# Kernel optimization log

Hardware: AMD Instinct MI355X
Metric: run time of the kernel (lower is better)

The kernel has to match this reference:

```python
import jax, jax.numpy as jnp
import numpy as np

N = 50000      # nodes
E = 800000     # edges (before self loops)
F_IN = 64      # n_features
H = 4          # heads
EPS = 1e-5


def _feast_conv(x, src, dst, W, u, c, b, out_ch):
    # FeaStConv (PyG): q_h = softmax_h(u_h^T (x_j - x_i) + c_h);
    # x_i' = mean_{j in N(i)} sum_h q_h * (W_h x_j) + b
    xs = x[src]                                   # [E', Fin]
    xd = x[dst]                                   # [E', Fin]
    q = jax.nn.softmax((xs - xd) @ u + c, axis=-1)          # [E', H]
    m = (xs @ W).reshape(xs.shape[0], H, out_ch)            # [E', H, out]
    msg = jnp.einsum('eh,eho->eo', q, m)                    # [E', out]
    num = jax.ops.segment_sum(msg, dst, num_segments=N)     # [N, out]
    deg = jax.ops.segment_sum(jnp.ones((msg.shape[0],), msg.dtype), dst, num_segments=N)
    return num / jnp.clip(deg, 1.0)[:, None] + b


def setup_inputs() -> dict:
    key = jax.random.key(0)
    ks = jax.random.split(key, 32)
    def gn(k, shape, s=0.1):
        return jax.random.normal(k, shape, jnp.float32) * s
    inp = {
        'x': jax.random.normal(ks[0], (N, F_IN), jnp.float32),
        'edge_index': jax.random.randint(ks[1], (2, E), 0, N),
        # FeaStConv 1: 64 -> 16
        'W1': gn(ks[2], (F_IN, H * 16)), 'u1': gn(ks[3], (F_IN, H)),
        'c1': gn(ks[4], (H,)), 'b1': gn(ks[5], (16,)),
        # FeaStConv 2: 16 -> 32
        'W2': gn(ks[6], (16, H * 32)), 'u2': gn(ks[7], (16, H)),
        'c2': gn(ks[8], (H,)), 'b2': gn(ks[9], (32,)),
        # FeaStConv 3: 32 -> 64
        'W3': gn(ks[10], (32, H * 64)), 'u3': gn(ks[11], (32, H)),
        'c3': gn(ks[12], (H,)), 'b3': gn(ks[13], (64,)),
        # BatchNorm(64) affine params (training-mode batch stats)
        'gamma': jnp.ones((64,), jnp.float32), 'beta': jnp.zeros((64,), jnp.float32),
        # MLP head
        'lw1': gn(ks[14], (64, 32)), 'lb1': gn(ks[15], (32,)),
        'lw2': gn(ks[16], (32, 16)), 'lb2': gn(ks[17], (16,)),
        'lw3': gn(ks[18], (16, 8)),  'lb3': gn(ks[19], (8,)),
        'lw4': gn(ks[20], (8, 4)),   'lb4': gn(ks[21], (4,)),
        'ow':  gn(ks[22], (4, 1)),   'ob':  gn(ks[23], (1,)),
    }
    return inp


def reference(x, edge_index, W1, u1, c1, b1, W2, u2, c2, b2, W3, u3, c3, b3,
              gamma, beta, lw1, lb1, lw2, lb2, lw3, lb3, lw4, lb4, ow, ob):
    # add self loops (PyG FeaStConv default)
    loops = jnp.arange(N, dtype=edge_index.dtype)
    src = jnp.concatenate([edge_index[0], loops])
    dst = jnp.concatenate([edge_index[1], loops])

    h = jax.nn.relu(_feast_conv(x, src, dst, W1, u1, c1, b1, 16))
    h = jax.nn.relu(_feast_conv(h, src, dst, W2, u2, c2, b2, 32))
    h = jax.nn.relu(_feast_conv(h, src, dst, W3, u3, c3, b3, 64))

    # BatchNorm over node dim (training-mode biased batch stats)
    mu = h.mean(axis=0)
    var = h.var(axis=0)
    h = (h - mu) * jax.lax.rsqrt(var + EPS) * gamma + beta

    h = jax.nn.relu(h @ lw1 + lb1)
    h = jax.nn.relu(h @ lw2 + lb2)
    h = jax.nn.relu(h @ lw3 + lb3)
    h = jax.nn.relu(h @ lw4 + lb4)
    return jax.nn.sigmoid(h @ ow + ob)    # [N, 1]
```

## Files before the change

### kernel.cpp

```cpp
#include <hip/hip_runtime.h>

#define NNODES 50000
#define NEDGES 800000
#define SCAN_BLOCKS ((NNODES + 255) / 256)
#define NPART (NNODES / 8)
#define EPS 2048
#define NSLICE ((NEDGES + EPS - 1) / EPS)

typedef unsigned short u16;

__device__ __forceinline__ float4 softq(float4 ss, float4 sd, float4 c4) {
  float l0 = ss.x - sd.x + c4.x;
  float l1 = ss.y - sd.y + c4.y;
  float l2 = ss.z - sd.z + c4.z;
  float l3 = ss.w - sd.w + c4.w;
  float mx = fmaxf(fmaxf(l0, l1), fmaxf(l2, l3));
  float e0 = __expf(l0 - mx), e1 = __expf(l1 - mx);
  float e2 = __expf(l2 - mx), e3 = __expf(l3 - mx);
  float inv = 1.f / (e0 + e1 + e2 + e3);
  return make_float4(e0 * inv, e1 * inv, e2 * inv, e3 * inv);
}

__device__ __forceinline__ void fma4(float4& a, float q, float4 v) {
  a.x += q * v.x; a.y += q * v.y; a.z += q * v.z; a.w += q * v.w;
}
__device__ __forceinline__ float dot4(float4 a, float4 b) {
  return a.x * b.x + a.y * b.y + a.z * b.z + a.w * b.w;
}
__device__ __forceinline__ void st4T(float* ldsT, int k0, int NBp, int nl, float4 v) {
  ldsT[(k0 + 0) * NBp + nl] = v.x;
  ldsT[(k0 + 1) * NBp + nl] = v.y;
  ldsT[(k0 + 2) * NBp + nl] = v.z;
  ldsT[(k0 + 3) * NBp + nl] = v.w;
}
__device__ __forceinline__ float4 shfl4(float4 v, int e, int w) {
  return make_float4(__shfl(v.x, e, w), __shfl(v.y, e, w),
                     __shfl(v.z, e, w), __shfl(v.w, e, w));
}

__global__ __launch_bounds__(256) void hist_kernel(const int* __restrict__ ei,
                                                   int* __restrict__ counts,
                                                   u16* __restrict__ rank) {
  int e = blockIdx.x * 256 + threadIdx.x;
  if (e < NEDGES) rank[e] = (u16)atomicAdd(&counts[ei[NEDGES + e]], 1);
}

__global__ __launch_bounds__(256) void scanA_kernel(const int* __restrict__ counts,
                                                    int* __restrict__ rowptr,
                                                    int* __restrict__ blockSum) {
  __shared__ int sm[256];
  int i = blockIdx.x * 256 + threadIdx.x;
  int v = (i < NNODES) ? counts[i] : 0;
  sm[threadIdx.x] = v;
  __syncthreads();
  for (int off = 1; off < 256; off <<= 1) {
    int x = (threadIdx.x >= off) ? sm[threadIdx.x - off] : 0;
    __syncthreads();
    sm[threadIdx.x] += x;
    __syncthreads();
  }
  if (i < NNODES) rowptr[i] = sm[threadIdx.x] - v;
  if (threadIdx.x == 255) blockSum[blockIdx.x] = sm[255];
}

__global__ __launch_bounds__(256) void scanBC_kernel(const int* __restrict__ blockSum,
                                                     int* __restrict__ rowptr) {
  __shared__ int sm[256];
  int v = (threadIdx.x < SCAN_BLOCKS) ? blockSum[threadIdx.x] : 0;
  sm[threadIdx.x] = v;
  __syncthreads();
  for (int off = 1; off < 256; off <<= 1) {
    int x = (threadIdx.x >= off) ? sm[threadIdx.x - off] : 0;
    __syncthreads();
    sm[threadIdx.x] += x;
    __syncthreads();
  }
  int off = (blockIdx.x == 0) ? 0 : sm[blockIdx.x - 1];
  int i = blockIdx.x * 256 + threadIdx.x;
  if (i < NNODES) rowptr[i] += off;
  if (i == 0) rowptr[NNODES] = NEDGES;
}

__global__ __launch_bounds__(256) void scatter_kernel(const int* __restrict__ ei,
                                                      const int* __restrict__ rowptr,
                                                      const u16* __restrict__ rank,
                                                      u16* __restrict__ col) {
  const int p = blockIdx.x & 7;
  const int sl = blockIdx.x >> 3;
  const int P0 = p * NPART;
  const int e1 = min((sl + 1) * EPS, NEDGES);
  for (int e = sl * EPS + threadIdx.x; e < e1; e += 256) {
    int dst = __builtin_nontemporal_load(&ei[NEDGES + e]);
    if ((unsigned)(dst - P0) < (unsigned)NPART) {
      int pos = rowptr[dst] + (int)__builtin_nontemporal_load(&rank[e]);
      col[pos] = (u16)__builtin_nontemporal_load(&ei[e]);
    }
  }
}

__global__ __launch_bounds__(256) void prep_kernel(const float* __restrict__ W1,
                                                   const float* __restrict__ W2,
                                                   const float* __restrict__ W3,
                                                   float* __restrict__ Wk1,
                                                   float* __restrict__ Wk2,
                                                   float* __restrict__ Wk3) {
  int i = blockIdx.x * 256 + threadIdx.x;
  if (i < 4096) {
    int f = i >> 6, j = i & 63;
    Wk1[i] = W1[f * 64 + ((j & 3) << 4) + (j >> 2)];
  } else if (i < 6144) {
    int i2 = i - 4096;
    int k = i2 >> 5, o = i2 & 31;
    int hh = k >> 4, f = k & 15;
    Wk2[i2] = W2[f * 128 + hh * 32 + o];
  } else if (i < 14336) {
    int i3 = i - 6144;
    int k = i3 >> 6, o = i3 & 63;
    int hh = k >> 5, f = k & 31;
    Wk3[i3] = W3[f * 256 + hh * 64 + o];
  }
}

template<int K, int OUTT, int MO>
__global__ __launch_bounds__(256) void ngemm_kernel(const float* __restrict__ A,
                                                    const float* __restrict__ Wk,
                                                    float* __restrict__ C) {
  constexpr int OG = OUTT / MO;
  constexpr int NB = 256 / OG;
  constexpr int NBp = NB + 1;
  __shared__ float ldsT[K * NBp];
  const int tid = threadIdx.x;
  const int nb0 = blockIdx.x * NB;
  for (int i = tid; i < NB * (K / 4); i += 256) {
    int r = i / (K / 4), kq = i - r * (K / 4);
    int n = nb0 + r;
    if (n >= NNODES) n = NNODES - 1;
    float4 v = ((const float4*)A)[n * (K / 4) + kq];
    st4T(ldsT, kq << 2, NBp, r, v);
  }
  __syncthreads();
  const int o0 = __builtin_amdgcn_readfirstlane(tid / NB) * MO;
  const int nl = tid & (NB - 1);
  const int n = nb0 + nl;
  float acc[MO];
#pragma unroll
  for (int m = 0; m < MO; ++m) acc[m] = 0.f;
#pragma unroll 4
  for (int k = 0; k < K; ++k) {
    float a = ldsT[k * NBp + nl];
    const float* wr = Wk + k * OUTT + o0;
#pragma unroll
    for (int m = 0; m < MO; ++m) acc[m] += a * wr[m];
  }
  if (n < NNODES) {
#pragma unroll
    for (int m4 = 0; m4 < MO / 4; ++m4) {
      float4 v = make_float4(acc[m4 * 4 + 0], acc[m4 * 4 + 1],
                             acc[m4 * 4 + 2], acc[m4 * 4 + 3]);
      ((float4*)C)[n * (OUTT / 4) + (o0 >> 2) + m4] = v;
    }
  }
}

template<int FIN, int OUTT, int MO>
__global__ __launch_bounds__(256) void fusedG_kernel(const int* __restrict__ rowptr,
                                                     const u16* __restrict__ col,
                                                     const float* __restrict__ s,
                                                     const float* __restrict__ x,
                                                     const float* __restrict__ Wk,
                                                     const float* __restrict__ cptr,
                                                     const float* __restrict__ bptr,
                                                     float* __restrict__ h) {
  constexpr int LPN = FIN / 8;
  constexpr int NB = 256 / LPN;
  constexpr int NBp = NB + 1;
  constexpr int K = 4 * FIN;
  constexpr int OG = OUTT / MO;
  static_assert(OG == 256 / NB, "geometry mismatch");
  __shared__ float ldsT[K * NBp];
  const int tid = threadIdx.x;
  const int nb0 = blockIdx.x * NB;
  const float4* sF4 = (const float4*)s;
  const float4* xF4 = (const float4*)x;

  {
    const int lane = tid & (LPN - 1);
    const int sub = tid / LPN;
    int n = nb0 + sub;
    if (n >= NNODES) n = NNODES - 1;
    float4 c4 = *(const float4*)cptr;
    float mxc = fmaxf(fmaxf(c4.x, c4.y), fmaxf(c4.z, c4.w));
    float4 qsl = make_float4(__expf(c4.x - mxc), __expf(c4.y - mxc),
                             __expf(c4.z - mxc), __expf(c4.w - mxc));
    float sinv = 1.f / (qsl.x + qsl.y + qsl.z + qsl.w);
    qsl.x *= sinv; qsl.y *= sinv; qsl.z *= sinv; qsl.w *= sinv;
    float4 sd = sF4[n];
    const float4* xn = xF4 + n * (FIN / 4) + 2 * lane;
    float4 xa = xn[0], xb = xn[1];
    float4 g0a = make_float4(qsl.x * xa.x, qsl.x * xa.y, qsl.x * xa.z, qsl.x * xa.w);
    float4 g0b = make_float4(qsl.x * xb.x, qsl.x * xb.y, qsl.x * xb.z, qsl.x * xb.w);
    float4 g1a = make_float4(qsl.y * xa.x, qsl.y * xa.y, qsl.y * xa.z, qsl.y * xa.w);
    float4 g1b = make_float4(qsl.y * xb.x, qsl.y * xb.y, qsl.y * xb.z, qsl.y * xb.w);
    float4 g2a = make_float4(qsl.z * xa.x, qsl.z * xa.y, qsl.z * xa.z, qsl.z * xa.w);
    float4 g2b = make_float4(qsl.z * xb.x, qsl.z * xb.y, qsl.z * xb.z, qsl.z * xb.w);
    float4 g3a = make_float4(qsl.w * xa.x, qsl.w * xa.y, qsl.w * xa.z, qsl.w * xa.w);
    float4 g3b = make_float4(qsl.w * xb.x, qsl.w * xb.y, qsl.w * xb.z, qsl.w * xb.w);
    const int beg = rowptr[n], end = rowptr[n + 1];
    int idx = beg;
    for (; idx + LPN <= end; idx += LPN) {
      int myS = (int)col[idx + lane];
      float4 qL = softq(sF4[myS], sd, c4);
#pragma unroll
      for (int e = 0; e < LPN; ++e) {
        int srcE = __shfl(myS, e, LPN);
        float4 q = shfl4(qL, e, LPN);
        const float4* xr = xF4 + srcE * (FIN / 4) + 2 * lane;
        float4 x0a = xr[0], x0b = xr[1];
        fma4(g0a, q.x, x0a); fma4(g0b, q.x, x0b);
        fma4(g1a, q.y, x0a); fma4(g1b, q.y, x0b);
        fma4(g2a, q.z, x0a); fma4(g2b, q.z, x0b);
        fma4(g3a, q.w, x0a); fma4(g3b, q.w, x0b);
      }
    }
    for (; idx < end; ++idx) {
      int s0 = (int)col[idx];
      float4 qv = softq(sF4[s0], sd, c4);
      const float4* xr = xF4 + s0 * (FIN / 4) + 2 * lane;
      float4 x0a = xr[0], x0b = xr[1];
      fma4(g0a, qv.x, x0a); fma4(g0b, qv.x, x0b);
      fma4(g1a, qv.y, x0a); fma4(g1b, qv.y, x0b);
      fma4(g2a, qv.z, x0a); fma4(g2b, qv.z, x0b);
      fma4(g3a, qv.w, x0a); fma4(g3b, qv.w, x0b);
    }
    const int f0 = 8 * lane;
    st4T(ldsT, 0 * FIN + f0, NBp, sub, g0a); st4T(ldsT, 0 * FIN + f0 + 4, NBp, sub, g0b);
    st4T(ldsT, 1 * FIN + f0, NBp, sub, g1a); st4T(ldsT, 1 * FIN + f0 + 4, NBp, sub, g1b);
    st4T(ldsT, 2 * FIN + f0, NBp, sub, g2a); st4T(ldsT, 2 * FIN + f0 + 4, NBp, sub, g2b);
    st4T(ldsT, 3 * FIN + f0, NBp, sub, g3a); st4T(ldsT, 3 * FIN + f0 + 4, NBp, sub, g3b);
  }
  __syncthreads();

  const int o0 = __builtin_amdgcn_readfirstlane(tid / NB) * MO;
  const int nl = tid & (NB - 1);
  const int n = nb0 + nl;
  float acc[MO];
#pragma unroll
  for (int m = 0; m < MO; ++m) acc[m] = 0.f;
#pragma unroll 4
  for (int k = 0; k < K; ++k) {
    float a = ldsT[k * NBp + nl];
    const float* wr = Wk + k * OUTT + o0;
#pragma unroll
    for (int m = 0; m < MO; ++m) acc[m] += a * wr[m];
  }
  if (n < NNODES) {
    float sc = 1.f / (float)(rowptr[n + 1] - rowptr[n] + 1);
#pragma unroll
    for (int m4 = 0; m4 < MO / 4; ++m4) {
      float4 v;
      v.x = fmaxf(acc[m4 * 4 + 0] * sc + bptr[o0 + m4 * 4 + 0], 0.f);
      v.y = fmaxf(acc[m4 * 4 + 1] * sc + bptr[o0 + m4 * 4 + 1], 0.f);
      v.z = fmaxf(acc[m4 * 4 + 2] * sc + bptr[o0 + m4 * 4 + 2], 0.f);
      v.w = fmaxf(acc[m4 * 4 + 3] * sc + bptr[o0 + m4 * 4 + 3], 0.f);
      ((float4*)h)[n * (OUTT / 4) + (o0 >> 2) + m4] = v;
    }
  }
}

template<int FIN>
__global__ __launch_bounds__(256) void s_kernel(const float* __restrict__ x,
                                                const float* __restrict__ u,
                                                float* __restrict__ s) {
  int tid = blockIdx.x * 256 + threadIdx.x;
  int n = tid >> 2, h = tid & 3;
  if (n >= NNODES) return;
  const float4* xr = (const float4*)x + n * (FIN / 4);
  float acc = 0.f;
#pragma unroll
  for (int f4 = 0; f4 < FIN / 4; ++f4) {
    float4 xv = xr[f4];
    acc += xv.x * u[(4 * f4 + 0) * 4 + h] + xv.y * u[(4 * f4 + 1) * 4 + h] +
           xv.z * u[(4 * f4 + 2) * 4 + h] + xv.w * u[(4 * f4 + 3) * 4 + h];
  }
  s[tid] = acc;
}

__global__ __launch_bounds__(256) void gather1_kernel(const int* __restrict__ rowptr,
                                                      const u16* __restrict__ col,
                                                      const float* __restrict__ s,
                                                      const float* __restrict__ t,
                                                      const float* __restrict__ cptr,
                                                      const float* __restrict__ bptr,
                                                      float* __restrict__ h) {
  const int lane = threadIdx.x & 7;
  const int sub = threadIdx.x >> 3;
  const int n = blockIdx.x * 32 + sub;
  if (n >= NNODES) return;
  const float4* sF4 = (const float4*)s;
  const float4* tF4 = (const float4*)t;
  float4 c4 = *(const float4*)cptr;
  float mxc = fmaxf(fmaxf(c4.x, c4.y), fmaxf(c4.z, c4.w));
  float4 qs = make_float4(__expf(c4.x - mxc), __expf(c4.y - mxc),
                          __expf(c4.z - mxc), __expf(c4.w - mxc));
  float sinv = 1.f / (qs.x + qs.y + qs.z + qs.w);
  qs.x *= sinv; qs.y *= sinv; qs.z *= sinv; qs.w *= sinv;
  float4 sd = sF4[n];
  const float4* trow = tF4 + n * 16 + 2 * lane;
  float acc0 = dot4(qs, trow[0]);
  float acc1 = dot4(qs, trow[1]);
  const int beg = rowptr[n], end = rowptr[n + 1];
  int idx = beg;
  for (; idx + 8 <= end; idx += 8) {
    int myS = (int)col[idx + lane];
    float4 qL = softq(sF4[myS], sd, c4);
#pragma unroll
    for (int e = 0; e < 8; ++e) {
      int srcE = __shfl(myS, e, 8);
      float4 q = shfl4(qL, e, 8);
      const float4* tw = tF4 + srcE * 16 + 2 * lane;
      acc0 += dot4(q, tw[0]);
      acc1 += dot4(q, tw[1]);
    }
  }
  for (; idx < end; ++idx) {
    int src = (int)col[idx];
    float4 qv = softq(sF4[src], sd, c4);
    const float4* tw = tF4 + src * 16 + 2 * lane;
    acc0 += dot4(qv, tw[0]);
    acc1 += dot4(qv, tw[1]);
  }
  float d = 1.f / (float)(end - beg + 1);
  h[n * 16 + 2 * lane + 0] = fmaxf(acc0 * d + bptr[2 * lane + 0], 0.f);
  h[n * 16 + 2 * lane + 1] = fmaxf(acc1 * d + bptr[2 * lane + 1], 0.f);
}

__global__ __launch_bounds__(256) void stats_kernel(const float* __restrict__ h3,
                                                    float* __restrict__ sums) {
  const int o = threadIdx.x & 63;
  const int r = threadIdx.x >> 6;
  float accS = 0.f, accQ = 0.f;
  for (int base = blockIdx.x * 4; base < NNODES; base += gridDim.x * 4) {
    int n = base + r;
    if (n < NNODES) {
      float v = h3[n * 64 + o];
      accS += v;
      accQ += v * v;
    }
  }
  __shared__ float ls[256], lq[256];
  ls[threadIdx.x] = accS;
  lq[threadIdx.x] = accQ;
  __syncthreads();
  if (threadIdx.x < 64) {
    float a = ls[threadIdx.x] + ls[threadIdx.x + 64] + ls[threadIdx.x + 128] + ls[threadIdx.x + 192];
    float qq = lq[threadIdx.x] + lq[threadIdx.x + 64] + lq[threadIdx.x + 128] + lq[threadIdx.x + 192];
    atomicAdd(&sums[threadIdx.x], a);
    atomicAdd(&sums[64 + threadIdx.x], qq);
  }
}

__global__ __launch_bounds__(256) void mlp_kernel(
    const float* __restrict__ h3, const float* __restrict__ sums,
    const float* __restrict__ gamma, const float* __restrict__ beta,
    const float* __restrict__ lw1, const float* __restrict__ lb1,
    const float* __restrict__ lw2, const float* __restrict__ lb2,
    const float* __restrict__ lw3, const float* __restrict__ lb3,
    const float* __restrict__ lw4, const float* __restrict__ lb4,
    const float* __restrict__ ow, const float* __restrict__ ob,
    float* __restrict__ out) {
  __shared__ float w1[64 * 32], w2[32 * 16], w3[16 * 8], w4[8 * 4];
  __shared__ float b1s[32], b2s[16], b3s[8], b4s[4], wos[4];
  __shared__ float scale[64], shift[64];
  int tid = threadIdx.x;
  for (int i = tid; i < 64 * 32; i += 256) w1[i] = lw1[i];
  for (int i = tid; i < 32 * 16; i += 256) w2[i] = lw2[i];
  if (tid < 128) w3[tid] = lw3[tid];
  if (tid < 32) { w4[tid] = lw4[tid]; b1s[tid] = lb1[tid]; }
  if (tid < 16) b2s[tid] = lb2[tid];
  if (tid < 8) b3s[tid] = lb3[tid];
  if (tid < 4) { b4s[tid] = lb4[tid]; wos[tid] = ow[tid]; }
  if (tid < 64) {
    float mu = sums[tid] * (1.f / NNODES);
    float var = sums[64 + tid] * (1.f / NNODES) - mu * mu;
    float sc = rsqrtf(var + 1e-5f) * gamma[tid];
    scale[tid] = sc;
    shift[tid] = beta[tid] - mu * sc;
  }
  __syncthreads();
  int n = blockIdx.x * 256 + tid;
  if (n >= NNODES) return;
  float obv = ob[0];
  const float4* hr = (const float4*)h3 + n * 16;
  float z1[32];
#pragma unroll
  for (int j = 0; j < 32; ++j) z1[j] = b1s[j];
  for (int i4 = 0; i4 < 16; ++i4) {
    float4 hv = hr[i4];
    float a0 = hv.x * scale[4 * i4 + 0] + shift[4 * i4 + 0];
    float a1 = hv.y * scale[4 * i4 + 1] + shift[4 * i4 + 1];
    float a2 = hv.z * scale[4 * i4 + 2] + shift[4 * i4 + 2];
    float a3 = hv.w * scale[4 * i4 + 3] + shift[4 * i4 + 3];
#pragma unroll
    for (int j = 0; j < 32; ++j) {
      z1[j] += a0 * w1[(4 * i4 + 0) * 32 + j] + a1 * w1[(4 * i4 + 1) * 32 + j] +
               a2 * w1[(4 * i4 + 2) * 32 + j] + a3 * w1[(4 * i4 + 3) * 32 + j];
    }
  }
  float z2[16];
#pragma unroll
  for (int j = 0; j < 16; ++j) z2[j] = b2s[j];
  for (int i = 0; i < 32; ++i) {
    float a = fmaxf(z1[i], 0.f);
#pragma unroll
    for (int j = 0; j < 16; ++j) z2[j] += a * w2[i * 16 + j];
  }
  float z3[8];
#pragma unroll
  for (int j = 0; j < 8; ++j) z3[j] = b3s[j];
  for (int i = 0; i < 16; ++i) {
    float a = fmaxf(z2[i], 0.f);
#pragma unroll
    for (int j = 0; j < 8; ++j) z3[j] += a * w3[i * 8 + j];
  }
  float z4[4];
#pragma unroll
  for (int j = 0; j < 4; ++j) z4[j] = b4s[j];
  for (int i = 0; i < 8; ++i) {
    float a = fmaxf(z3[i], 0.f);
#pragma unroll
    for (int j = 0; j < 4; ++j) z4[j] += a * w4[i * 4 + j];
  }
  float zo = obv;
#pragma unroll
  for (int i = 0; i < 4; ++i) zo += fmaxf(z4[i], 0.f) * wos[i];
  out[n] = 1.f / (1.f + __expf(-zo));
}

extern "C" void kernel_launch(void* const* d_in, const int* in_sizes, int n_in,
                              void* d_out, int out_size, void* d_ws, size_t ws_size,
                              hipStream_t stream) {
  const float* x  = (const float*)d_in[0];
  const int*   ei = (const int*)d_in[1];
  const float* W1 = (const float*)d_in[2];  const float* u1 = (const float*)d_in[3];
  const float* c1 = (const float*)d_in[4];  const float* b1 = (const float*)d_in[5];
  const float* W2 = (const float*)d_in[6];  const float* u2 = (const float*)d_in[7];
  const float* c2 = (const float*)d_in[8];  const float* b2 = (const float*)d_in[9];
  const float* W3 = (const float*)d_in[10]; const float* u3 = (const float*)d_in[11];
  const float* c3 = (const float*)d_in[12]; const float* b3 = (const float*)d_in[13];
  const float* gamma = (const float*)d_in[14]; const float* beta = (const float*)d_in[15];
  const float* lw1 = (const float*)d_in[16]; const float* lb1 = (const float*)d_in[17];
  const float* lw2 = (const float*)d_in[18]; const float* lb2 = (const float*)d_in[19];
  const float* lw3 = (const float*)d_in[20]; const float* lb3 = (const float*)d_in[21];
  const float* lw4 = (const float*)d_in[22]; const float* lb4 = (const float*)d_in[23];
  const float* ow  = (const float*)d_in[24]; const float* ob  = (const float*)d_in[25];
  float* out = (float*)d_out;

  float* t    = (float*)d_ws;
  float* hA   = t + (size_t)NNODES * 64;
  float* hB   = hA + (size_t)NNODES * 64;
  float* s    = hB + (size_t)NNODES * 64;
  float* sums = s + (size_t)NNODES * 4;
  float* Wk1  = sums + 128;
  float* Wk2  = Wk1 + 4096;
  float* Wk3  = Wk2 + 2048;
  int*   rowptr   = (int*)(Wk3 + 8192);
  int*   counts   = rowptr + NNODES + 8;
  int*   blockSum = counts + NNODES;
  u16*   col      = (u16*)(blockSum + 256);
  u16*   rank     = col + NEDGES;

  hipMemsetAsync(counts, 0, NNODES * sizeof(int), stream);
  hipMemsetAsync(sums, 0, 128 * sizeof(float), stream);

  prep_kernel<<<56, 256, 0, stream>>>(W1, W2, W3, Wk1, Wk2, Wk3);
  hist_kernel<<<(NEDGES + 255) / 256, 256, 0, stream>>>(ei, counts, rank);
  scanA_kernel<<<SCAN_BLOCKS, 256, 0, stream>>>(counts, rowptr, blockSum);
  scanBC_kernel<<<SCAN_BLOCKS, 256, 0, stream>>>(blockSum, rowptr);
  scatter_kernel<<<NSLICE * 8, 256, 0, stream>>>(ei, rowptr, rank, col);

  ngemm_kernel<64, 64, 16><<<(NNODES + 63) / 64, 256, 0, stream>>>(x, Wk1, t);
  s_kernel<64><<<(NNODES * 4 + 255) / 256, 256, 0, stream>>>(x, u1, s);
  gather1_kernel<<<(NNODES + 31) / 32, 256, 0, stream>>>(rowptr, col, s, t, c1, b1, hA);

  s_kernel<16><<<(NNODES * 4 + 255) / 256, 256, 0, stream>>>(hA, u2, s);
  fusedG_kernel<16, 32, 16><<<(NNODES + 127) / 128, 256, 0, stream>>>(
      rowptr, col, s, hA, Wk2, c2, b2, hB);

  s_kernel<32><<<(NNODES * 4 + 255) / 256, 256, 0, stream>>>(hB, u3, s);
  fusedG_kernel<32, 64, 16><<<(NNODES + 63) / 64, 256, 0, stream>>>(
      rowptr, col, s, hB, Wk3, c3, b3, hA);

  stats_kernel<<<256, 256, 0, stream>>>(hA, sums);
  mlp_kernel<<<(NNODES + 255) / 256, 256, 0, stream>>>(hA, sums, gamma, beta, lw1, lb1,
                                                       lw2, lb2, lw3, lb3, lw4, lb4,
                                                       ow, ob, out);
}
```

Measured before the change: 237.2 us.

## Fuse weight prep into histogram, fold attention projections into GEMM and gather

Merges the weight-permutation prep kernel into the edge histogram kernel and moves the zeroing of the stats buffer into the first scan kernel, dropping one launch and one memset. The layer-1 attention projection x@u1 is computed inside the node GEMM from the already-staged LDS tile. The layer-2 projection h1@u2 is computed in the gather1 epilogue with a shuffle reduction across the 8 lanes that own a node. This removes two s_kernel launches and their re-reads of x and h1. It uses separate sA and sB buffers to avoid aliasing, and adds a little work to the GEMM and gather kernels.

```diff
diff --git a/kernel.cpp b/kernel.cpp
--- a/kernel.cpp
+++ b/kernel.cpp
@@ -38,72 +38,15 @@
                      __shfl(v.z, e, w), __shfl(v.w, e, w));
 }
 
-__global__ __launch_bounds__(256) void hist_kernel(const int* __restrict__ ei,
-                                                   int* __restrict__ counts,
-                                                   u16* __restrict__ rank) {
-  int e = blockIdx.x * 256 + threadIdx.x;
-  if (e < NEDGES) rank[e] = (u16)atomicAdd(&counts[ei[NEDGES + e]], 1);
-}
-
-__global__ __launch_bounds__(256) void scanA_kernel(const int* __restrict__ counts,
-                                                    int* __restrict__ rowptr,
-                                                    int* __restrict__ blockSum) {
-  __shared__ int sm[256];
-  int i = blockIdx.x * 256 + threadIdx.x;
-  int v = (i < NNODES) ? counts[i] : 0;
-  sm[threadIdx.x] = v;
-  __syncthreads();
-  for (int off = 1; off < 256; off <<= 1) {
-    int x = (threadIdx.x >= off) ? sm[threadIdx.x - off] : 0;
-    __syncthreads();
-    sm[threadIdx.x] += x;
-    __syncthreads();
-  }
-  if (i < NNODES) rowptr[i] = sm[threadIdx.x] - v;
-  if (threadIdx.x == 255) blockSum[blockIdx.x] = sm[255];
-}
-
-__global__ __launch_bounds__(256) void scanBC_kernel(const int* __restrict__ blockSum,
-                                                     int* __restrict__ rowptr) {
-  __shared__ int sm[256];
-  int v = (threadIdx.x < SCAN_BLOCKS) ? blockSum[threadIdx.x] : 0;
-  sm[threadIdx.x] = v;
-  __syncthreads();
-  for (int off = 1; off < 256; off <<= 1) {
-    int x = (threadIdx.x >= off) ? sm[threadIdx.x - off] : 0;
-    __syncthreads();
-    sm[threadIdx.x] += x;
-    __syncthreads();
-  }
-  int off = (blockIdx.x == 0) ? 0 : sm[blockIdx.x - 1];
-  int i = blockIdx.x * 256 + threadIdx.x;
-  if (i < NNODES) rowptr[i] += off;
-  if (i == 0) rowptr[NNODES] = NEDGES;
-}
-
-__global__ __launch_bounds__(256) void scatter_kernel(const int* __restrict__ ei,
-                                                      const int* __restrict__ rowptr,
-                                                      const u16* __restrict__ rank,
-                                                      u16* __restrict__ col) {
-  const int p = blockIdx.x & 7;
-  const int sl = blockIdx.x >> 3;
-  const int P0 = p * NPART;
-  const int e1 = min((sl + 1) * EPS, NEDGES);
-  for (int e = sl * EPS + threadIdx.x; e < e1; e += 256) {
-    int dst = __builtin_nontemporal_load(&ei[NEDGES + e]);
-    if ((unsigned)(dst - P0) < (unsigned)NPART) {
-      int pos = rowptr[dst] + (int)__builtin_nontemporal_load(&rank[e]);
-      col[pos] = (u16)__builtin_nontemporal_load(&ei[e]);
-    }
-  }
-}
-
-__global__ __launch_bounds__(256) void prep_kernel(const float* __restrict__ W1,
-                                                   const float* __restrict__ W2,
-                                                   const float* __restrict__ W3,
-                                                   float* __restrict__ Wk1,
-                                                   float* __restrict__ Wk2,
-                                                   float* __restrict__ Wk3) {
+__global__ __launch_bounds__(256) void histprep_kernel(const int* __restrict__ ei,
+                                                       int* __restrict__ counts,
+                                                       u16* __restrict__ rank,
+                                                       const float* __restrict__ W1,
+                                                       const float* __restrict__ W2,
+                                                       const float* __restrict__ W3,
+                                                       float* __restrict__ Wk1,
+                                                       float* __restrict__ Wk2,
+                                                       float* __restrict__ Wk3) {
   int i = blockIdx.x * 256 + threadIdx.x;
   if (i < 4096) {
     int f = i >> 6, j = i & 63;
@@ -119,12 +62,70 @@
     int hh = k >> 5, f = k & 31;
     Wk3[i3] = W3[f * 256 + hh * 64 + o];
   }
-}
-
-template<int K, int OUTT, int MO>
-__global__ __launch_bounds__(256) void ngemm_kernel(const float* __restrict__ A,
-                                                    const float* __restrict__ Wk,
-                                                    float* __restrict__ C) {
+  if (i < NEDGES) rank[i] = (u16)atomicAdd(&counts[ei[NEDGES + i]], 1);
+}
+
+__global__ __launch_bounds__(256) void scanA_kernel(const int* __restrict__ counts,
+                                                    int* __restrict__ rowptr,
+                                                    int* __restrict__ blockSum,
+                                                    float* __restrict__ sums) {
+  if (blockIdx.x == 0 && threadIdx.x < 128) sums[threadIdx.x] = 0.f;
+  __shared__ int sm[256];
+  int i = blockIdx.x * 256 + threadIdx.x;
+  int v = (i < NNODES) ? counts[i] : 0;
+  sm[threadIdx.x] = v;
+  __syncthreads();
+  for (int off = 1; off < 256; off <<= 1) {
+    int x = (threadIdx.x >= off) ? sm[threadIdx.x - off] : 0;
+    __syncthreads();
+    sm[threadIdx.x] += x;
+    __syncthreads();
+  }
+  if (i < NNODES) rowptr[i] = sm[threadIdx.x] - v;
+  if (threadIdx.x == 255) blockSum[blockIdx.x] = sm[255];
+}
+
+__global__ __launch_bounds__(256) void scanBC_kernel(const int* __restrict__ blockSum,
+                                                     int* __restrict__ rowptr) {
+  __shared__ int sm[256];
+  int v = (threadIdx.x < SCAN_BLOCKS) ? blockSum[threadIdx.x] : 0;
+  sm[threadIdx.x] = v;
+  __syncthreads();
+  for (int off = 1; off < 256; off <<= 1) {
+    int x = (threadIdx.x >= off) ? sm[threadIdx.x - off] : 0;
+    __syncthreads();
+    sm[threadIdx.x] += x;
+    __syncthreads();
+  }
+  int off = (blockIdx.x == 0) ? 0 : sm[blockIdx.x - 1];
+  int i = blockIdx.x * 256 + threadIdx.x;
+  if (i < NNODES) rowptr[i] += off;
+  if (i == 0) rowptr[NNODES] = NEDGES;
+}
+
+__global__ __launch_bounds__(256) void scatter_kernel(const int* __restrict__ ei,
+                                                      const int* __restrict__ rowptr,
+                                                      const u16* __restrict__ rank,
+                                                      u16* __restrict__ col) {
+  const int p = blockIdx.x & 7;
+  const int sl = blockIdx.x >> 3;
+  const int P0 = p * NPART;
+  const int e1 = min((sl + 1) * EPS, NEDGES);
+  for (int e = sl * EPS + threadIdx.x; e < e1; e += 256) {
+    int dst = __builtin_nontemporal_load(&ei[NEDGES + e]);
+    if ((unsigned)(dst - P0) < (unsigned)NPART) {
+      int pos = rowptr[dst] + (int)__builtin_nontemporal_load(&rank[e]);
+      col[pos] = (u16)__builtin_nontemporal_load(&ei[e]);
+    }
+  }
+}
+
+__global__ __launch_bounds__(256) void ngemm1_kernel(const float* __restrict__ A,
+                                                     const float* __restrict__ Wk,
+                                                     const float* __restrict__ u1,
+                                                     float* __restrict__ t,
+                                                     float* __restrict__ sOut) {
+  constexpr int K = 64, OUTT = 64, MO = 16;
   constexpr int OG = OUTT / MO;
   constexpr int NB = 256 / OG;
   constexpr int NBp = NB + 1;
@@ -157,8 +158,16 @@
     for (int m4 = 0; m4 < MO / 4; ++m4) {
       float4 v = make_float4(acc[m4 * 4 + 0], acc[m4 * 4 + 1],
                              acc[m4 * 4 + 2], acc[m4 * 4 + 3]);
-      ((float4*)C)[n * (OUTT / 4) + (o0 >> 2) + m4] = v;
-    }
+      ((float4*)t)[n * (OUTT / 4) + (o0 >> 2) + m4] = v;
+    }
+  }
+  {
+    const int hh = __builtin_amdgcn_readfirstlane(tid >> 6);
+    float accs = 0.f;
+#pragma unroll 4
+    for (int k = 0; k < K; ++k)
+      accs += ldsT[k * NBp + nl] * u1[k * 4 + hh];
+    if (n < NNODES) sOut[n * 4 + hh] = accs;
   }
 }
 
@@ -291,7 +300,9 @@
                                                       const float* __restrict__ t,
                                                       const float* __restrict__ cptr,
                                                       const float* __restrict__ bptr,
-                                                      float* __restrict__ h) {
+                                                      const float* __restrict__ u2,
+                                                      float* __restrict__ h,
+                                                      float* __restrict__ sOut) {
   const int lane = threadIdx.x & 7;
   const int sub = threadIdx.x >> 3;
   const int n = blockIdx.x * 32 + sub;
@@ -330,8 +341,22 @@
     acc1 += dot4(qv, tw[1]);
   }
   float d = 1.f / (float)(end - beg + 1);
-  h[n * 16 + 2 * lane + 0] = fmaxf(acc0 * d + bptr[2 * lane + 0], 0.f);
-  h[n * 16 + 2 * lane + 1] = fmaxf(acc1 * d + bptr[2 * lane + 1], 0.f);
+  float v0 = fmaxf(acc0 * d + bptr[2 * lane + 0], 0.f);
+  float v1 = fmaxf(acc1 * d + bptr[2 * lane + 1], 0.f);
+  h[n * 16 + 2 * lane + 0] = v0;
+  h[n * 16 + 2 * lane + 1] = v1;
+  float4 ua = ((const float4*)u2)[2 * lane];
+  float4 ub = ((const float4*)u2)[2 * lane + 1];
+  float4 p = make_float4(v0 * ua.x + v1 * ub.x, v0 * ua.y + v1 * ub.y,
+                         v0 * ua.z + v1 * ub.z, v0 * ua.w + v1 * ub.w);
+#pragma unroll
+  for (int off = 1; off < 8; off <<= 1) {
+    p.x += __shfl_xor(p.x, off);
+    p.y += __shfl_xor(p.y, off);
+    p.z += __shfl_xor(p.z, off);
+    p.w += __shfl_xor(p.w, off);
+  }
+  if (lane == 0) ((float4*)sOut)[n] = p;
 }
 
 __global__ __launch_bounds__(256) void stats_kernel(const float* __restrict__ h3,
@@ -458,8 +483,9 @@
   float* t    = (float*)d_ws;
   float* hA   = t + (size_t)NNODES * 64;
   float* hB   = hA + (size_t)NNODES * 64;
-  float* s    = hB + (size_t)NNODES * 64;
-  float* sums = s + (size_t)NNODES * 4;
+  float* sA   = hB + (size_t)NNODES * 64;
+  float* sB   = sA + (size_t)NNODES * 4;
+  float* sums = sB + (size_t)NNODES * 4;
   float* Wk1  = sums + 128;
   float* Wk2  = Wk1 + 4096;
   float* Wk3  = Wk2 + 2048;
@@ -470,25 +496,23 @@
   u16*   rank     = col + NEDGES;
 
   hipMemsetAsync(counts, 0, NNODES * sizeof(int), stream);
-  hipMemsetAsync(sums, 0, 128 * sizeof(float), stream);
-
-  prep_kernel<<<56, 256, 0, stream>>>(W1, W2, W3, Wk1, Wk2, Wk3);
-  hist_kernel<<<(NEDGES + 255) / 256, 256, 0, stream>>>(ei, counts, rank);
-  scanA_kernel<<<SCAN_BLOCKS, 256, 0, stream>>>(counts, rowptr, blockSum);
+
+  histprep_kernel<<<(NEDGES + 255) / 256, 256, 0, stream>>>(ei, counts, rank,
+                                                            W1, W2, W3, Wk1, Wk2, Wk3);
+  scanA_kernel<<<SCAN_BLOCKS, 256, 0, stream>>>(counts, rowptr, blockSum, sums);
   scanBC_kernel<<<SCAN_BLOCKS, 256, 0, stream>>>(blockSum, rowptr);
   scatter_kernel<<<NSLICE * 8, 256, 0, stream>>>(ei, rowptr, rank, col);
 
-  ngemm_kernel<64, 64, 16><<<(NNODES + 63) / 64, 256, 0, stream>>>(x, Wk1, t);
-  s_kernel<64><<<(NNODES * 4 + 255) / 256, 256, 0, stream>>>(x, u1, s);
-  gather1_kernel<<<(NNODES + 31) / 32, 256, 0, stream>>>(rowptr, col, s, t, c1, b1, hA);
-
-  s_kernel<16><<<(NNODES * 4 + 255) / 256, 256, 0, stream>>>(hA, u2, s);
+  ngemm1_kernel<<<(NNODES + 63) / 64, 256, 0, stream>>>(x, Wk1, u1, t, sA);
+  gather1_kernel<<<(NNODES + 31) / 32, 256, 0, stream>>>(rowptr, col, sA, t, c1, b1,
+                                                         u2, hA, sB);
+
   fusedG_kernel<16, 32, 16><<<(NNODES + 127) / 128, 256, 0, stream>>>(
-      rowptr, col, s, hA, Wk2, c2, b2, hB);
-
-  s_kernel<32><<<(NNODES * 4 + 255) / 256, 256, 0, stream>>>(hB, u3, s);
+      rowptr, col, sB, hA, Wk2, c2, b2, hB);
+
+  s_kernel<32><<<(NNODES * 4 + 255) / 256, 256, 0, stream>>>(hB, u3, sA);
   fusedG_kernel<32, 64, 16><<<(NNODES + 63) / 64, 256, 0, stream>>>(
-      rowptr, col, s, hB, Wk3, c3, b3, hA);
+      rowptr, col, sA, hB, Wk3, c3, b3, hA);
 
   stats_kernel<<<256, 256, 0, stream>>>(hA, sums);
   mlp_kernel<<<(NNODES + 255) / 256, 256, 0, stream>>>(hA, sums, gamma, beta, lw1, lb1,
```

Result: faster. 225.4 us (-4.9%).
